# Kernel optimization log

Hardware: AMD Instinct MI355X
Metric: run time of the kernel (lower is better)

The kernel has to match this reference:

```python
import jax, jax.numpy as jnp
import numpy as np
from jax import lax

BATCH = 512
FS = 24        # filter_size
QDIM = 11      # sort-of-clevr question vector length
IMG = 80       # 80 -> 40 -> 20 -> 10 -> 5 via four stride-2 convs
D = 5
OBJ = D * D    # 25 objects
PAIR_IN = (FS + 2) * 2 + QDIM  # 63
HID = 256
EPS = 1e-5


def setup_inputs() -> dict:
    key = jax.random.key(0)
    ks = jax.random.split(key, 24)

    def n(k, shape, s=0.05):
        return jax.random.normal(k, shape, jnp.float32) * s

    inp = {
        "img": jax.random.normal(ks[0], (BATCH, 3, IMG, IMG), jnp.float32),
        "qst": jax.random.normal(ks[1], (QDIM, BATCH), jnp.float32),
    }
    chans = [3, FS, FS, FS]
    ki = 2
    for l in range(4):
        inp[f"cw{l+1}"] = n(ks[ki], (FS, chans[l], 3, 3)); ki += 1
        inp[f"cb{l+1}"] = jnp.zeros((FS,), jnp.float32)
        inp[f"bg{l+1}"] = jnp.ones((FS,), jnp.float32)
        inp[f"bb{l+1}"] = jnp.zeros((FS,), jnp.float32)
    g_in = [PAIR_IN, HID, HID, HID]
    for l in range(4):
        inp[f"g{l+1}w"] = n(ks[ki], (HID, g_in[l])); ki += 1
        inp[f"g{l+1}b"] = jnp.zeros((HID,), jnp.float32)
    inp["f1w"] = n(ks[ki], (HID, HID)); ki += 1
    inp["f1b"] = jnp.zeros((HID,), jnp.float32)
    inp["fc2w"] = n(ks[ki], (HID, HID)); ki += 1
    inp["fc2b"] = jnp.zeros((HID,), jnp.float32)
    inp["fc3w"] = n(ks[ki], (10, HID)); ki += 1
    inp["fc3b"] = jnp.zeros((10,), jnp.float32)
    return inp


def _conv_bn(x, w, b, gamma, beta):
    # conv stride 2, pad 1 -> relu -> batchnorm (training-mode batch stats)
    y = lax.conv_general_dilated(x, w, (2, 2), [(1, 1), (1, 1)],
                                 dimension_numbers=("NCHW", "OIHW", "NCHW"))
    y = jax.nn.relu(y + b[None, :, None, None])
    mean = y.mean(axis=(0, 2, 3))
    var = y.var(axis=(0, 2, 3))
    inv = gamma * lax.rsqrt(var + EPS)
    return (y - mean[None, :, None, None]) * inv[None, :, None, None] + beta[None, :, None, None]


def _lin(x, w, b):
    return x @ w.T + b


def reference(img, qst,
              cw1, cb1, bg1, bb1, cw2, cb2, bg2, bb2,
              cw3, cb3, bg3, bb3, cw4, cb4, bg4, bb4,
              g1w, g1b, g2w, g2b, g3w, g3b, g4w, g4b,
              f1w, f1b, fc2w, fc2b, fc3w, fc3b):
    q = qst.T  # [mb, QDIM] (torch.transpose(qst,0,1).float())

    x = _conv_bn(img, cw1, cb1, bg1, bb1)
    x = _conv_bn(x, cw2, cb2, bg2, bb2)
    x = _conv_bn(x, cw3, cb3, bg3, bb3)
    x = _conv_bn(x, cw4, cb4, bg4, bb4)   # [mb, FS, 5, 5]

    mb = x.shape[0]
    x_flat = x.reshape(mb, FS, OBJ).transpose(0, 2, 1)  # [mb, 25, FS]

    idx = jnp.arange(OBJ)
    coord = jnp.stack([(idx // 5 - 2) / 2.0, (idx % 5 - 2) / 2.0], axis=-1).astype(jnp.float32)
    x_flat = jnp.concatenate([x_flat, jnp.broadcast_to(coord, (mb, OBJ, 2))], axis=2)  # [mb,25,FS+2]

    # pair[b, k, i] = concat(obj_i, obj_k, q)  (matches torch x_i/x_j/cat layout)
    oi = jnp.broadcast_to(x_flat[:, None, :, :], (mb, OBJ, OBJ, FS + 2))
    oj = jnp.broadcast_to(x_flat[:, :, None, :], (mb, OBJ, OBJ, FS + 2))
    qq = jnp.broadcast_to(q[:, None, None, :], (mb, OBJ, OBJ, QDIM))
    pairs = jnp.concatenate([oi, oj, qq], axis=3).reshape(mb * OBJ * OBJ, PAIR_IN)

    h = jax.nn.relu(_lin(pairs, g1w, g1b))
    h = jax.nn.relu(_lin(h, g2w, g2b))
    h = jax.nn.relu(_lin(h, g3w, g3b))
    h = jax.nn.relu(_lin(h, g4w, g4b))
    x_g = h.reshape(mb, OBJ * OBJ, HID).sum(axis=1)  # [mb, 256]

    x_f = jax.nn.relu(_lin(x_g, f1w, f1b))
    x_f = jax.nn.relu(_lin(x_f, fc2w, fc2b))
    # dropout treated as identity (eval-mode deterministic reference)
    logits = _lin(x_f, fc3w, fc3b)
    return jax.nn.log_softmax(logits, axis=-1)
```

## Files before the change

kernel.cpp:

```cpp
#include <hip/hip_runtime.h>
#include <math.h>

#define MB    512
#define FS    24
#define QDIM  11
#define OBJ   25
#define HID   256

typedef unsigned short u16;
typedef __attribute__((ext_vector_type(8))) __bf16 bf16x8;
typedef __attribute__((ext_vector_type(4))) float f32x4;

__device__ __forceinline__ float bf2f(u16 h) {
    return __uint_as_float(((unsigned int)h) << 16);
}
__device__ __forceinline__ u16 f2bf(float f) {
    unsigned int u = __float_as_uint(f);
    return (u16)((u + 0x7FFFu + ((u >> 16) & 1u)) >> 16);
}

__global__ __launch_bounds__(256) void prep_all(
    const float* __restrict__ g2w, const float* __restrict__ g3w,
    const float* __restrict__ g4w, u16* __restrict__ wfrag,
    const float* __restrict__ cw1, const float* __restrict__ cw2,
    const float* __restrict__ cw3, const float* __restrict__ cw4,
    float* __restrict__ wt1, u16* __restrict__ wcfrag)
{
    if (blockIdx.x < 768) {
        int idx = blockIdx.x * 256 + threadIdx.x;
        int jj = idx & 7;
        int lane = (idx >> 3) & 63;
        int tn = (idx >> 9) & 15;
        int c = (idx >> 13) & 7;
        int l = idx >> 16;
        const float* W = (l == 0) ? g2w : ((l == 1) ? g3w : g4w);
        int n = tn * 16 + (lane & 15);
        int k = c * 32 + (lane >> 4) * 8 + jj;
        wfrag[idx] = f2bf(W[n * 256 + k]);
    } else {
        int idx = (blockIdx.x - 768) * 256 + threadIdx.x;
        if (idx < 648) {
            int k = idx / 24, oc = idx % 24;
            wt1[idx] = cw1[oc * 27 + k];
        } else if (idx < 648 + 27648) {
            int t = idx - 648;
            int l = t / 9216, r = t % 9216;
            int cell = r / 1024, rr = r % 1024;
            int o = rr / 512, q = rr % 512;
            int lane = q / 8, j = q % 8;
            int oc = o * 16 + (lane & 15);
            int ic = (lane >> 4) * 8 + j;
            const float* w = (l == 0) ? cw2 : ((l == 1) ? cw3 : cw4);
            u16 v = 0;
            if (oc < 24 && ic < 24) v = f2bf(w[oc * 216 + ic * 9 + cell]);
            wcfrag[t] = v;
        }
    }
}

__global__ __launch_bounds__(256) void conv1_t(
    const float* __restrict__ img, const float* __restrict__ wt1,
    const float* __restrict__ bias, float* __restrict__ yout,
    float* __restrict__ stats)
{
    __shared__ float tile[3 * 21 * 85];
    __shared__ float wS[648];
    __shared__ float part[48];
    const int tid = threadIdx.x;
    const int b   = blockIdx.x >> 2;
    const int y0  = (blockIdx.x & 3) * 10;
    const int iy_base = 2 * y0 - 1;
    for (int e = tid; e < 648; e += 256) wS[e] = wt1[e];
    for (int e = tid; e < 3 * 21 * 85; e += 256) {
        int ixt = e % 85; int rem = e / 85;
        int iyl = rem % 21; int ic = rem / 21;
        int iy = iy_base + iyl, ix = ixt - 1;
        float v = 0.f;
        if ((unsigned)iy < 80u && (unsigned)ix < 80u)
            v = img[((size_t)(b * 3 + ic) * 80 + iy) * 80 + ix];
        tile[e] = v;
    }
    if (tid < 48) part[tid] = 0.f;
    __syncthreads();

    float rsum[24], rsq[24];
#pragma unroll
    for (int oc = 0; oc < 24; oc++) { rsum[oc] = 0.f; rsq[oc] = 0.f; }

#pragma unroll 1
    for (int pp = 0; pp < 2; pp++) {
        const int pxl = tid + pp * 256;
        const bool active = pxl < 400;
        const int pxc = active ? pxl : 0;
        const int yl = pxc / 40, x = pxc % 40;
        float acc[24];
#pragma unroll
        for (int oc = 0; oc < 24; oc++) acc[oc] = bias[oc];
#pragma unroll 1
        for (int ic = 0; ic < 3; ic++) {
#pragma unroll 1
            for (int ky = 0; ky < 3; ky++) {
#pragma unroll 1
                for (int kx = 0; kx < 3; kx++) {
                    const int k = (ic * 3 + ky) * 3 + kx;
                    float xin = tile[ic * 1785 + (2 * yl + ky) * 85 + (2 * x + kx)];
                    const float4* wrow = (const float4*)&wS[k * 24];
#pragma unroll
                    for (int g = 0; g < 6; g++) {
                        float4 wv = wrow[g];
                        acc[g * 4 + 0] = fmaf(xin, wv.x, acc[g * 4 + 0]);
                        acc[g * 4 + 1] = fmaf(xin, wv.y, acc[g * 4 + 1]);
                        acc[g * 4 + 2] = fmaf(xin, wv.z, acc[g * 4 + 2]);
                        acc[g * 4 + 3] = fmaf(xin, wv.w, acc[g * 4 + 3]);
                    }
                }
            }
        }
#pragma unroll
        for (int oc = 0; oc < 24; oc++)
            acc[oc] = active ? fmaxf(acc[oc], 0.f) : 0.f;
        if (active) {
            float* op = &yout[((size_t)b * 1600 + (y0 + yl) * 40 + x) * 24];
#pragma unroll
            for (int g = 0; g < 6; g++)
                *(float4*)&op[g * 4] = make_float4(acc[g * 4], acc[g * 4 + 1],
                                                   acc[g * 4 + 2], acc[g * 4 + 3]);
        }
#pragma unroll
        for (int oc = 0; oc < 24; oc++) {
            rsum[oc] += acc[oc];
            rsq[oc]  += acc[oc] * acc[oc];
        }
    }
#pragma unroll
    for (int oc = 0; oc < 24; oc++) {
        float a = rsum[oc], q = rsq[oc];
#pragma unroll
        for (int off = 1; off < 64; off <<= 1) {
            a += __shfl_xor(a, off, 64);
            q += __shfl_xor(q, off, 64);
        }
        if ((tid & 63) == 0) { atomicAdd(&part[oc], a); atomicAdd(&part[24 + oc], q); }
    }
    __syncthreads();
    if (tid < 48) atomicAdd(&stats[tid], part[tid]);
}

template<int HIN, int HOUT, int YT, int MT>
__global__ __launch_bounds__(256) void convM(
    const float* __restrict__ yin,
    const float* __restrict__ stp, const float* __restrict__ gam,
    const float* __restrict__ bet, float invN,
    const u16* __restrict__ wcf_g,
    const float* __restrict__ bias,
    float* __restrict__ yout, float* __restrict__ stats)
{
    constexpr int ROWS = 2 * YT + 1;
    constexpr int R    = 2 * HOUT + 1;
    constexpr int POS  = ROWS * R;
    constexpr int NPX  = HOUT * HOUT;
    constexpr int NPXB = YT * HOUT;
    constexpr int TILES = HOUT / YT;
    constexpr int MTPW = (MT + 3) / 4;
    __shared__ __align__(16) u16 tile[POS * 24 + 16];
    __shared__ float scW[48];
    __shared__ float part[48];
    const int tid  = threadIdx.x;
    const int b    = (TILES == 1) ? blockIdx.x : (int)(blockIdx.x / TILES);
    const int y0   = (TILES == 1) ? 0 : (int)(blockIdx.x % TILES) * YT;
    const int lane = tid & 63, wave = tid >> 6;
    const int r16  = lane & 15, quad = lane >> 4;

    if (tid < 24) {
        float m   = stp[tid] * invN;
        float var = stp[24 + tid] * invN - m * m;
        float inv = gam[tid] * rsqrtf(var + 1e-5f);
        scW[tid]      = inv;
        scW[24 + tid] = bet[tid] - m * inv;
    }
    if (tid < 48) part[tid] = 0.f;

    bf16x8 wcf[9][2];
#pragma unroll
    for (int c = 0; c < 9; c++)
#pragma unroll
        for (int o = 0; o < 2; o++)
            wcf[c][o] = *(const bf16x8*)&wcf_g[((c * 2 + o) * 64 + lane) * 8];

    __syncthreads();

    const int iy_base = 2 * y0 - 1;
    for (int p = tid; p < POS; p += 256) {
        int iyl = p / R, ixt = p % R;
        int iy = iy_base + iyl, ix = ixt - 1;
        u16 hv[24];
        if ((unsigned)iy < (unsigned)HIN && (unsigned)ix < (unsigned)HIN) {
            const float* ip = &yin[((size_t)b * HIN * HIN + iy * HIN + ix) * 24];
#pragma unroll
            for (int c = 0; c < 24; c++)
                hv[c] = f2bf(ip[c] * scW[c] + scW[24 + c]);
        } else {
#pragma unroll
            for (int c = 0; c < 24; c++) hv[c] = 0;
        }
#pragma unroll
        for (int g = 0; g < 3; g++)
            *(uint4*)&tile[p * 24 + g * 8] = *(uint4*)&hv[g * 8];
    }
    __syncthreads();

    f32x4 acc[MTPW][2];
#pragma unroll
    for (int t = 0; t < MTPW; t++) {
        acc[t][0] = (f32x4)(0.f);
        acc[t][1] = (f32x4)(0.f);
    }

    int baseT[MTPW];
#pragma unroll
    for (int t = 0; t < MTPW; t++) {
        int mt = wave + t * 4;
        int pxl = mt * 16 + r16;
        if (pxl > NPXB - 1) pxl = NPXB - 1;
        baseT[t] = ((2 * (pxl / HOUT)) * R + 2 * (pxl % HOUT)) * 24 + quad * 8;
    }

#pragma unroll
    for (int ky = 0; ky < 3; ky++) {
#pragma unroll
        for (int kx = 0; kx < 3; kx++) {
            const int cell = ky * 3 + kx;
            const int coff = (ky * R + kx) * 24;
            bf16x8 xf[MTPW];
#pragma unroll
            for (int t = 0; t < MTPW; t++) {
                int mt = wave + t * 4;
                uint4 tmp = make_uint4(0, 0, 0, 0);
                if (mt < MT && quad < 3)
                    tmp = *(const uint4*)&tile[baseT[t] + coff];
                xf[t] = *(bf16x8*)&tmp;
            }
#pragma unroll
            for (int t = 0; t < MTPW; t++) {
                int mt = wave + t * 4;
                if (mt < MT) {
                    acc[t][0] = __builtin_amdgcn_mfma_f32_16x16x32_bf16(
                        wcf[cell][0], xf[t], acc[t][0], 0, 0, 0);
                    acc[t][1] = __builtin_amdgcn_mfma_f32_16x16x32_bf16(
                        wcf[cell][1], xf[t], acc[t][1], 0, 0, 0);
                }
            }
        }
    }

    float ss[2][4], qq[2][4];
#pragma unroll
    for (int o = 0; o < 2; o++)
#pragma unroll
        for (int r = 0; r < 4; r++) { ss[o][r] = 0.f; qq[o][r] = 0.f; }

#pragma unroll
    for (int t = 0; t < MTPW; t++) {
        int mt = wave + t * 4;
        if (mt >= MT) continue;
        int pxl = mt * 16 + r16;
        bool pv = pxl < NPXB;
        int pxi = y0 * HOUT + pxl;
#pragma unroll
        for (int o = 0; o < 2; o++) {
            int ocb = o * 16 + quad * 4;
            if (pv && ocb < 24) {
                float4 bb = *(const float4*)&bias[ocb];
                float v0 = fmaxf(acc[t][o][0] + bb.x, 0.f);
                float v1 = fmaxf(acc[t][o][1] + bb.y, 0.f);
                float v2 = fmaxf(acc[t][o][2] + bb.z, 0.f);
                float v3 = fmaxf(acc[t][o][3] + bb.w, 0.f);
                *(float4*)&yout[((size_t)b * NPX + pxi) * 24 + ocb] =
                    make_float4(v0, v1, v2, v3);
                ss[o][0] += v0; qq[o][0] += v0 * v0;
                ss[o][1] += v1; qq[o][1] += v1 * v1;
                ss[o][2] += v2; qq[o][2] += v2 * v2;
                ss[o][3] += v3; qq[o][3] += v3 * v3;
            }
        }
    }
#pragma unroll
    for (int o = 0; o < 2; o++) {
        int ocb = o * 16 + quad * 4;
#pragma unroll
        for (int r = 0; r < 4; r++) {
            float a = ss[o][r], q = qq[o][r];
            a += __shfl_xor(a, 1, 64); q += __shfl_xor(q, 1, 64);
            a += __shfl_xor(a, 2, 64); q += __shfl_xor(q, 2, 64);
            a += __shfl_xor(a, 4, 64); q += __shfl_xor(q, 4, 64);
            a += __shfl_xor(a, 8, 64); q += __shfl_xor(q, 8, 64);
            if (r16 == 0 && ocb < 24) {
                atomicAdd(&part[ocb + r], a);
                atomicAdd(&part[24 + ocb + r], q);
            }
        }
    }
    __syncthreads();
    if (tid < 48) atomicAdd(&stats[tid], part[tid]);
}

__global__ __launch_bounds__(256) void uv_kernel(
    const float* __restrict__ y4t,
    const float* __restrict__ stp, const float* __restrict__ gam,
    const float* __restrict__ bet, float invN,
    const float* __restrict__ qst, const float* __restrict__ g1w,
    const float* __restrict__ g1b, u16* __restrict__ u, u16* __restrict__ v)
{
    int b = blockIdx.x, tid = threadIdx.x;
    __shared__ float xf[650];
    __shared__ float qv[11];
    __shared__ float scW[48];
    if (tid < 24) {
        float m   = stp[tid] * invN;
        float var = stp[24 + tid] * invN - m * m;
        float inv = gam[tid] * rsqrtf(var + 1e-5f);
        scW[tid]      = inv;
        scW[24 + tid] = bet[tid] - m * inv;
    }
    __syncthreads();
    for (int e = tid; e < 650; e += 256) {
        int o = e / 26, c = e % 26;
        float val;
        if (c < 24)      val = y4t[b * 600 + o * 24 + c] * scW[c] + scW[24 + c];
        else if (c == 24) val = (float)(o / 5 - 2) * 0.5f;
        else              val = (float)(o % 5 - 2) * 0.5f;
        xf[e] = val;
    }
    if (tid < 11) qv[tid] = qst[tid * MB + b];
    __syncthreads();
    const int n = tid;
    float wrow[63];
#pragma unroll
    for (int c = 0; c < 63; c++) wrow[c] = g1w[n * 63 + c];
    float qsum = g1b[n];
#pragma unroll
    for (int j = 0; j < 11; j++) qsum += wrow[52 + j] * qv[j];
    for (int o = 0; o < 25; o++) {
        float uu = 0.f, vv = qsum;
#pragma unroll
        for (int c = 0; c < 26; c++) {
            uu += wrow[c]      * xf[o * 26 + c];
            vv += wrow[26 + c] * xf[o * 26 + c];
        }
        u[(b * 25 + o) * 256 + n] = f2bf(uu);
        v[(b * 25 + o) * 256 + n] = f2bf(vv);
    }
}

__global__ __launch_bounds__(256, 2) void g_fused(
    const u16* __restrict__ u_bf, const u16* __restrict__ v_bf,
    const u16* __restrict__ wfrag,
    const float* __restrict__ b2, const float* __restrict__ b3, const float* __restrict__ b4,
    float* __restrict__ xg)
{
    __shared__ u16 hS[32768];
    const int tid  = threadIdx.x;
    const int b    = blockIdx.x / 5;
    const int p0   = (blockIdx.x % 5) * 128;
    const int lane = tid & 63, wave = tid >> 6;
    const int r16  = lane & 15, sub = lane >> 4;
    const int n0w  = wave * 64;

    const u16* wfL = wfrag + (size_t)(wave * 4) * 512 + (size_t)lane * 8;

    bf16x8 wcur[4], wnxt[4];
#pragma unroll
    for (int tn = 0; tn < 4; tn++)
        wcur[tn] = *(const bf16x8*)&wfL[(size_t)tn * 512];
#pragma unroll
    for (int tn = 0; tn < 4; tn++) wnxt[tn] = wcur[tn];

    {
        const int m = tid & 127, half = tid >> 7;
        const int p = p0 + m;
        if (p < 625) {
            const int oi = p % 25, ok = p / 25;
            const uint4* up = (const uint4*)(u_bf + (size_t)(b * 25 + oi) * 256);
            const uint4* vp = (const uint4*)(v_bf + (size_t)(b * 25 + ok) * 256);
#pragma unroll
            for (int gi = 0; gi < 16; gi++) {
                const int g = half * 16 + gi;
                uint4 ua = up[g], va = vp[g];
                const u16* uh = (const u16*)&ua;
                const u16* vh = (const u16*)&va;
                u16 o[8];
#pragma unroll
                for (int i = 0; i < 8; i++) {
                    float f = bf2f(uh[i]) + bf2f(vh[i]);
                    f = f > 0.f ? f : 0.f;
                    o[i] = f2bf(f);
                }
                *(uint4*)&hS[m * 256 + ((g ^ (m & 7)) * 8)] = *(uint4*)o;
            }
        } else {
            uint4 z = make_uint4(0, 0, 0, 0);
#pragma unroll
            for (int gi = 0; gi < 16; gi++) {
                const int g = half * 16 + gi;
                *(uint4*)&hS[m * 256 + ((g ^ (m & 7)) * 8)] = z;
            }
        }
    }

#pragma unroll 1
    for (int l = 0; l < 3; l++) {
        f32x4 acc[8][4];
#pragma unroll
        for (int tm = 0; tm < 8; tm++)
#pragma unroll
            for (int tn = 0; tn < 4; tn++)
                acc[tm][tn] = (f32x4)(0.f);

        __syncthreads();

#pragma unroll 1
        for (int kb = 0; kb < 8; kb++) {
            const int s = l * 8 + kb;
            if (s < 23) {
#pragma unroll
                for (int tn = 0; tn < 4; tn++)
                    wnxt[tn] = *(const bf16x8*)&wfL[((size_t)(s + 1) * 16 + tn) * 512];
            }
            bf16x8 bfr[8];
            const int g = kb * 4 + sub;
#pragma unroll
            for (int tm = 0; tm < 8; tm++) {
                const int m = tm * 16 + r16;
                bfr[tm] = *(const bf16x8*)&hS[m * 256 + ((g ^ (m & 7)) * 8)];
            }
#pragma unroll
            for (int tm = 0; tm < 8; tm++)
#pragma unroll
                for (int tn = 0; tn < 4; tn++)
                    acc[tm][tn] = __builtin_amdgcn_mfma_f32_16x16x32_bf16(
                        wcur[tn], bfr[tm], acc[tm][tn], 0, 0, 0);
#pragma unroll
            for (int tn = 0; tn < 4; tn++) wcur[tn] = wnxt[tn];
        }
        __syncthreads();

        const float* bl = (l == 0) ? b2 : ((l == 1) ? b3 : b4);
        if (l < 2) {
#pragma unroll
            for (int tn = 0; tn < 4; tn++) {
                const int n0 = n0w + tn * 16 + sub * 4;
                const float4 bb = *(const float4*)&bl[n0];
                const int gg = n0 >> 3;
                const int sh = (sub & 1) * 4;
#pragma unroll
                for (int tm = 0; tm < 8; tm++) {
                    const int m = tm * 16 + r16;
                    u16 o[4];
                    o[0] = f2bf(fmaxf(acc[tm][tn][0] + bb.x, 0.f));
                    o[1] = f2bf(fmaxf(acc[tm][tn][1] + bb.y, 0.f));
                    o[2] = f2bf(fmaxf(acc[tm][tn][2] + bb.z, 0.f));
                    o[3] = f2bf(fmaxf(acc[tm][tn][3] + bb.w, 0.f));
                    *(ushort4*)&hS[m * 256 + ((gg ^ (m & 7)) * 8) + sh] = *(ushort4*)o;
                }
            }
        } else {
            float s[4][4];
#pragma unroll
            for (int tn = 0; tn < 4; tn++)
#pragma unroll
                for (int r = 0; r < 4; r++) s[tn][r] = 0.f;
#pragma unroll
            for (int tn = 0; tn < 4; tn++) {
                const int n0 = n0w + tn * 16 + sub * 4;
                const float4 bb = *(const float4*)&bl[n0];
#pragma unroll
                for (int tm = 0; tm < 8; tm++) {
                    const int m = tm * 16 + r16;
                    if (p0 + m < 625) {
                        s[tn][0] += fmaxf(acc[tm][tn][0] + bb.x, 0.f);
                        s[tn][1] += fmaxf(acc[tm][tn][1] + bb.y, 0.f);
                        s[tn][2] += fmaxf(acc[tm][tn][2] + bb.z, 0.f);
                        s[tn][3] += fmaxf(acc[tm][tn][3] + bb.w, 0.f);
                    }
                }
            }
#pragma unroll
            for (int tn = 0; tn < 4; tn++)
#pragma unroll
                for (int r = 0; r < 4; r++) {
                    float v = s[tn][r];
                    v += __shfl_xor(v, 1, 64);
                    v += __shfl_xor(v, 2, 64);
                    v += __shfl_xor(v, 4, 64);
                    v += __shfl_xor(v, 8, 64);
                    if (r16 == 0)
                        atomicAdd(&xg[b * 256 + n0w + tn * 16 + sub * 4 + r], v);
                }
        }
    }
}

__global__ __launch_bounds__(256) void f_fused(
    const float* __restrict__ xg,
    const float* __restrict__ f1w, const float* __restrict__ f1b,
    const float* __restrict__ fc2w, const float* __restrict__ fc2b,
    const float* __restrict__ fc3w, const float* __restrict__ fc3b,
    float* __restrict__ out)
{
    const int b = blockIdx.x, tid = threadIdx.x;
    __shared__ float xa[256], xb[256], lg[10], red[2];
    xa[tid] = xg[b * 256 + tid];
    __syncthreads();
    {
        const float4* wr = (const float4*)(f1w + (size_t)tid * 256);
        float a = f1b[tid];
#pragma unroll
        for (int k4 = 0; k4 < 64; k4++) {
            float4 w4 = wr[k4];
            a += w4.x * xa[k4 * 4 + 0] + w4.y * xa[k4 * 4 + 1]
               + w4.z * xa[k4 * 4 + 2] + w4.w * xa[k4 * 4 + 3];
        }
        xb[tid] = a > 0.f ? a : 0.f;
    }
    __syncthreads();
    {
        const float4* wr = (const float4*)(fc2w + (size_t)tid * 256);
        float a = fc2b[tid];
#pragma unroll
        for (int k4 = 0; k4 < 64; k4++) {
            float4 w4 = wr[k4];
            a += w4.x * xb[k4 * 4 + 0] + w4.y * xb[k4 * 4 + 1]
               + w4.z * xb[k4 * 4 + 2] + w4.w * xb[k4 * 4 + 3];
        }
        __syncthreads();
        xa[tid] = a > 0.f ? a : 0.f;
    }
    __syncthreads();
    if (tid < 10) {
        const float4* wr = (const float4*)(fc3w + (size_t)tid * 256);
        float a = fc3b[tid];
#pragma unroll
        for (int k4 = 0; k4 < 64; k4++) {
            float4 w4 = wr[k4];
            a += w4.x * xa[k4 * 4 + 0] + w4.y * xa[k4 * 4 + 1]
               + w4.z * xa[k4 * 4 + 2] + w4.w * xa[k4 * 4 + 3];
        }
        lg[tid] = a;
    }
    __syncthreads();
    if (tid == 0) {
        float mx = lg[0];
        for (int o = 1; o < 10; o++) mx = lg[o] > mx ? lg[o] : mx;
        float ssum = 0.f;
        for (int o = 0; o < 10; o++) ssum += expf(lg[o] - mx);
        red[0] = mx;
        red[1] = logf(ssum);
    }
    __syncthreads();
    if (tid < 10) out[b * 10 + tid] = lg[tid] - red[0] - red[1];
}

extern "C" void kernel_launch(void* const* d_in, const int* in_sizes, int n_in,
                              void* d_out, int out_size, void* d_ws, size_t ws_size,
                              hipStream_t stream)
{
    const float* img  = (const float*)d_in[0];
    const float* qst  = (const float*)d_in[1];
    const float* cw1  = (const float*)d_in[2];
    const float* cb1  = (const float*)d_in[3];
    const float* bg1  = (const float*)d_in[4];
    const float* bb1  = (const float*)d_in[5];
    const float* cw2  = (const float*)d_in[6];
    const float* cb2  = (const float*)d_in[7];
    const float* bg2  = (const float*)d_in[8];
    const float* bb2  = (const float*)d_in[9];
    const float* cw3  = (const float*)d_in[10];
    const float* cb3  = (const float*)d_in[11];
    const float* bg3  = (const float*)d_in[12];
    const float* bb3  = (const float*)d_in[13];
    const float* cw4  = (const float*)d_in[14];
    const float* cb4  = (const float*)d_in[15];
    const float* bg4  = (const float*)d_in[16];
    const float* bb4  = (const float*)d_in[17];
    const float* g1w  = (const float*)d_in[18];
    const float* g1b  = (const float*)d_in[19];
    const float* g2w  = (const float*)d_in[20];
    const float* g2b  = (const float*)d_in[21];
    const float* g3w  = (const float*)d_in[22];
    const float* g3b  = (const float*)d_in[23];
    const float* g4w  = (const float*)d_in[24];
    const float* g4b  = (const float*)d_in[25];
    const float* f1w  = (const float*)d_in[26];
    const float* f1b  = (const float*)d_in[27];
    const float* fc2w = (const float*)d_in[28];
    const float* fc2b = (const float*)d_in[29];
    const float* fc3w = (const float*)d_in[30];
    const float* fc3b = (const float*)d_in[31];
    float* out = (float*)d_out;

    float* ws    = (float*)d_ws;
    float* stats = ws;
    float* xg    = ws + 192;
    u16*   wfrag = (u16*)(ws + 131456);
    float* y1    = ws + 328064;
    float* y2    = ws + 19988864;
    float* y3    = ws + 24904064;
    float* y4    = ws + 26132864;
    u16*   u_bf  = (u16*)(ws + 26440064);
    u16*   v_bf  = (u16*)(ws + 28078464);
    float* wt1   = ws + 29716864;
    u16*   wcfrag = (u16*)(ws + 29717512);

    hipMemsetAsync(stats, 0, (size_t)131264 * sizeof(float), stream);

    prep_all<<<879, 256, 0, stream>>>(g2w, g3w, g4w, wfrag,
                                      cw1, cw2, cw3, cw4, wt1, wcfrag);

    conv1_t<<<2048, 256, 0, stream>>>(img, wt1, cb1, y1, stats);

    convM<40, 20, 4, 5><<<2560, 256, 0, stream>>>(
        y1, stats, bg1, bb1, 1.f / 819200.f, wcfrag, cb2, y2, stats + 48);
    convM<20, 10, 10, 7><<<512, 256, 0, stream>>>(
        y2, stats + 48, bg2, bb2, 1.f / 204800.f, wcfrag + 9216, cb3, y3, stats + 96);
    convM<10, 5, 5, 2><<<512, 256, 0, stream>>>(
        y3, stats + 96, bg3, bb3, 1.f / 51200.f, wcfrag + 18432, cb4, y4, stats + 144);

    uv_kernel<<<512, 256, 0, stream>>>(y4, stats + 144, bg4, bb4, 1.f / 12800.f,
                                       qst, g1w, g1b, u_bf, v_bf);

    g_fused<<<2560, 256, 0, stream>>>(u_bf, v_bf, wfrag, g2b, g3b, g4b, xg);

    f_fused<<<512, 256, 0, stream>>>(xg, f1w, f1b, fc2w, fc2b, fc3w, fc3b, out);
}
```

Before: 492.8 us.

## Keep u/v in fp32, truncate-pack bf16 via perm, double-buffer weight fragments

Stores the first-layer u/v projections in fp32 instead of bf16 and sums them in fp32 before converting, moving rounding later at the cost of twice the traffic for u/v reads. Replaces round-to-nearest bf16 conversion with a single byte-permute truncation when packing pairs in the conv tile staging and g_fused hidden writes, cutting ALU work but changing rounding mode. Restructures the g_fused k-loop into an unrolled-by-two ping-pong of weight fragment registers, reloading per layer, to overlap global weight loads with MFMA. Workspace offsets are reshuffled to fit the larger buffers.

```diff
diff --git a/kernel.cpp b/kernel.cpp
--- a/kernel.cpp
+++ b/kernel.cpp
@@ -17,6 +17,9 @@
 __device__ __forceinline__ u16 f2bf(float f) {
     unsigned int u = __float_as_uint(f);
     return (u16)((u + 0x7FFFu + ((u >> 16) & 1u)) >> 16);
+}
+__device__ __forceinline__ unsigned pk2bf(float hi, float lo) {
+    return __builtin_amdgcn_perm(__float_as_uint(hi), __float_as_uint(lo), 0x07060302u);
 }
 
 __global__ __launch_bounds__(256) void prep_all(
@@ -193,19 +196,24 @@
     for (int p = tid; p < POS; p += 256) {
         int iyl = p / R, ixt = p % R;
         int iy = iy_base + iyl, ix = ixt - 1;
-        u16 hv[24];
+        unsigned w[12];
         if ((unsigned)iy < (unsigned)HIN && (unsigned)ix < (unsigned)HIN) {
             const float* ip = &yin[((size_t)b * HIN * HIN + iy * HIN + ix) * 24];
+            float e[24];
 #pragma unroll
             for (int c = 0; c < 24; c++)
-                hv[c] = f2bf(ip[c] * scW[c] + scW[24 + c]);
+                e[c] = fmaf(ip[c], scW[c], scW[24 + c]);
+#pragma unroll
+            for (int i = 0; i < 12; i++)
+                w[i] = pk2bf(e[2 * i + 1], e[2 * i]);
         } else {
 #pragma unroll
-            for (int c = 0; c < 24; c++) hv[c] = 0;
+            for (int i = 0; i < 12; i++) w[i] = 0;
         }
 #pragma unroll
         for (int g = 0; g < 3; g++)
-            *(uint4*)&tile[p * 24 + g * 8] = *(uint4*)&hv[g * 8];
+            *(uint4*)&tile[p * 24 + g * 8] =
+                make_uint4(w[g * 4], w[g * 4 + 1], w[g * 4 + 2], w[g * 4 + 3]);
     }
     __syncthreads();
 
@@ -309,7 +317,7 @@
     const float* __restrict__ stp, const float* __restrict__ gam,
     const float* __restrict__ bet, float invN,
     const float* __restrict__ qst, const float* __restrict__ g1w,
-    const float* __restrict__ g1b, u16* __restrict__ u, u16* __restrict__ v)
+    const float* __restrict__ g1b, float* __restrict__ u, float* __restrict__ v)
 {
     int b = blockIdx.x, tid = threadIdx.x;
     __shared__ float xf[650];
@@ -347,13 +355,13 @@
             uu += wrow[c]      * xf[o * 26 + c];
             vv += wrow[26 + c] * xf[o * 26 + c];
         }
-        u[(b * 25 + o) * 256 + n] = f2bf(uu);
-        v[(b * 25 + o) * 256 + n] = f2bf(vv);
+        u[(b * 25 + o) * 256 + n] = uu;
+        v[(b * 25 + o) * 256 + n] = vv;
     }
 }
 
 __global__ __launch_bounds__(256, 2) void g_fused(
-    const u16* __restrict__ u_bf, const u16* __restrict__ v_bf,
+    const float* __restrict__ u_f, const float* __restrict__ v_f,
     const u16* __restrict__ wfrag,
     const float* __restrict__ b2, const float* __restrict__ b3, const float* __restrict__ b4,
     float* __restrict__ xg)
@@ -368,34 +376,24 @@
 
     const u16* wfL = wfrag + (size_t)(wave * 4) * 512 + (size_t)lane * 8;
 
-    bf16x8 wcur[4], wnxt[4];
-#pragma unroll
-    for (int tn = 0; tn < 4; tn++)
-        wcur[tn] = *(const bf16x8*)&wfL[(size_t)tn * 512];
-#pragma unroll
-    for (int tn = 0; tn < 4; tn++) wnxt[tn] = wcur[tn];
-
     {
         const int m = tid & 127, half = tid >> 7;
         const int p = p0 + m;
         if (p < 625) {
             const int oi = p % 25, ok = p / 25;
-            const uint4* up = (const uint4*)(u_bf + (size_t)(b * 25 + oi) * 256);
-            const uint4* vp = (const uint4*)(v_bf + (size_t)(b * 25 + ok) * 256);
+            const float4* up = (const float4*)(u_f + (size_t)(b * 25 + oi) * 256);
+            const float4* vp = (const float4*)(v_f + (size_t)(b * 25 + ok) * 256);
 #pragma unroll
             for (int gi = 0; gi < 16; gi++) {
                 const int g = half * 16 + gi;
-                uint4 ua = up[g], va = vp[g];
-                const u16* uh = (const u16*)&ua;
-                const u16* vh = (const u16*)&va;
-                u16 o[8];
-#pragma unroll
-                for (int i = 0; i < 8; i++) {
-                    float f = bf2f(uh[i]) + bf2f(vh[i]);
-                    f = f > 0.f ? f : 0.f;
-                    o[i] = f2bf(f);
-                }
-                *(uint4*)&hS[m * 256 + ((g ^ (m & 7)) * 8)] = *(uint4*)o;
+                float4 ua = up[g * 2],     va = vp[g * 2];
+                float4 ub = up[g * 2 + 1], vb = vp[g * 2 + 1];
+                float f0 = fmaxf(ua.x + va.x, 0.f), f1 = fmaxf(ua.y + va.y, 0.f);
+                float f2 = fmaxf(ua.z + va.z, 0.f), f3 = fmaxf(ua.w + va.w, 0.f);
+                float f4 = fmaxf(ub.x + vb.x, 0.f), f5 = fmaxf(ub.y + vb.y, 0.f);
+                float f6 = fmaxf(ub.z + vb.z, 0.f), f7 = fmaxf(ub.w + vb.w, 0.f);
+                *(uint4*)&hS[m * 256 + ((g ^ (m & 7)) * 8)] =
+                    make_uint4(pk2bf(f1, f0), pk2bf(f3, f2), pk2bf(f5, f4), pk2bf(f7, f6));
             }
         } else {
             uint4 z = make_uint4(0, 0, 0, 0);
@@ -416,31 +414,56 @@
             for (int tn = 0; tn < 4; tn++)
                 acc[tm][tn] = (f32x4)(0.f);
 
+        bf16x8 wA[4], wB[4];
+#pragma unroll
+        for (int tn = 0; tn < 4; tn++)
+            wA[tn] = *(const bf16x8*)&wfL[((size_t)(l * 8) * 16 + tn) * 512];
+
         __syncthreads();
 
 #pragma unroll 1
-        for (int kb = 0; kb < 8; kb++) {
+        for (int kb = 0; kb < 8; kb += 2) {
             const int s = l * 8 + kb;
-            if (s < 23) {
+            if (s + 1 < 24) {
 #pragma unroll
                 for (int tn = 0; tn < 4; tn++)
-                    wnxt[tn] = *(const bf16x8*)&wfL[((size_t)(s + 1) * 16 + tn) * 512];
-            }
-            bf16x8 bfr[8];
-            const int g = kb * 4 + sub;
-#pragma unroll
-            for (int tm = 0; tm < 8; tm++) {
-                const int m = tm * 16 + r16;
-                bfr[tm] = *(const bf16x8*)&hS[m * 256 + ((g ^ (m & 7)) * 8)];
-            }
-#pragma unroll
-            for (int tm = 0; tm < 8; tm++)
+                    wB[tn] = *(const bf16x8*)&wfL[((size_t)(s + 1) * 16 + tn) * 512];
+            }
+            {
+                bf16x8 bfr[8];
+                const int g = kb * 4 + sub;
+#pragma unroll
+                for (int tm = 0; tm < 8; tm++) {
+                    const int m = tm * 16 + r16;
+                    bfr[tm] = *(const bf16x8*)&hS[m * 256 + ((g ^ (m & 7)) * 8)];
+                }
+#pragma unroll
+                for (int tm = 0; tm < 8; tm++)
+#pragma unroll
+                    for (int tn = 0; tn < 4; tn++)
+                        acc[tm][tn] = __builtin_amdgcn_mfma_f32_16x16x32_bf16(
+                            wA[tn], bfr[tm], acc[tm][tn], 0, 0, 0);
+            }
+            if (s + 2 < 24) {
 #pragma unroll
                 for (int tn = 0; tn < 4; tn++)
-                    acc[tm][tn] = __builtin_amdgcn_mfma_f32_16x16x32_bf16(
-                        wcur[tn], bfr[tm], acc[tm][tn], 0, 0, 0);
-#pragma unroll
-            for (int tn = 0; tn < 4; tn++) wcur[tn] = wnxt[tn];
+                    wA[tn] = *(const bf16x8*)&wfL[((size_t)(s + 2) * 16 + tn) * 512];
+            }
+            {
+                bf16x8 bfr[8];
+                const int g = (kb + 1) * 4 + sub;
+#pragma unroll
+                for (int tm = 0; tm < 8; tm++) {
+                    const int m = tm * 16 + r16;
+                    bfr[tm] = *(const bf16x8*)&hS[m * 256 + ((g ^ (m & 7)) * 8)];
+                }
+#pragma unroll
+                for (int tm = 0; tm < 8; tm++)
+#pragma unroll
+                    for (int tn = 0; tn < 4; tn++)
+                        acc[tm][tn] = __builtin_amdgcn_mfma_f32_16x16x32_bf16(
+                            wB[tn], bfr[tm], acc[tm][tn], 0, 0, 0);
+            }
         }
         __syncthreads();
 
@@ -455,12 +478,12 @@
 #pragma unroll
                 for (int tm = 0; tm < 8; tm++) {
                     const int m = tm * 16 + r16;
-                    u16 o[4];
-                    o[0] = f2bf(fmaxf(acc[tm][tn][0] + bb.x, 0.f));
-                    o[1] = f2bf(fmaxf(acc[tm][tn][1] + bb.y, 0.f));
-                    o[2] = f2bf(fmaxf(acc[tm][tn][2] + bb.z, 0.f));
-                    o[3] = f2bf(fmaxf(acc[tm][tn][3] + bb.w, 0.f));
-                    *(ushort4*)&hS[m * 256 + ((gg ^ (m & 7)) * 8) + sh] = *(ushort4*)o;
+                    float v0 = fmaxf(acc[tm][tn][0] + bb.x, 0.f);
+                    float v1 = fmaxf(acc[tm][tn][1] + bb.y, 0.f);
+                    float v2 = fmaxf(acc[tm][tn][2] + bb.z, 0.f);
+                    float v3 = fmaxf(acc[tm][tn][3] + bb.w, 0.f);
+                    uint2 pw = make_uint2(pk2bf(v1, v0), pk2bf(v3, v2));
+                    *(uint2*)&hS[m * 256 + ((gg ^ (m & 7)) * 8) + sh] = pw;
                 }
             }
         } else {
@@ -602,14 +625,14 @@
     float* stats = ws;
     float* xg    = ws + 192;
     u16*   wfrag = (u16*)(ws + 131456);
+    float* wt1   = ws + 229760;
+    u16*   wcfrag = (u16*)(ws + 230408);
     float* y1    = ws + 328064;
     float* y2    = ws + 19988864;
     float* y3    = ws + 24904064;
     float* y4    = ws + 26132864;
-    u16*   u_bf  = (u16*)(ws + 26440064);
-    u16*   v_bf  = (u16*)(ws + 28078464);
-    float* wt1   = ws + 29716864;
-    u16*   wcfrag = (u16*)(ws + 29717512);
+    float* u_f   = ws + 26440064;
+    float* v_f   = ws + 29716864;
 
     hipMemsetAsync(stats, 0, (size_t)131264 * sizeof(float), stream);
 
@@ -626,9 +649,9 @@
         y3, stats + 96, bg3, bb3, 1.f / 51200.f, wcfrag + 18432, cb4, y4, stats + 144);
 
     uv_kernel<<<512, 256, 0, stream>>>(y4, stats + 144, bg4, bb4, 1.f / 12800.f,
-                                       qst, g1w, g1b, u_bf, v_bf);
-
-    g_fused<<<2560, 256, 0, stream>>>(u_bf, v_bf, wfrag, g2b, g3b, g4b, xg);
+                                       qst, g1w, g1b, u_f, v_f);
+
+    g_fused<<<2560, 256, 0, stream>>>(u_f, v_f, wfrag, g2b, g3b, g4b, xg);
 
     f_fused<<<512, 256, 0, stream>>>(xg, f1w, f1b, fc2w, fc2b, fc3w, fc3b, out);
 }
```

Result: slower. 539.4 us (+9.5%).
